# Kernel tuning notes

Hardware: AMD Instinct MI355X
Metric: run time of the kernel (lower is better)

The kernel has to match this reference:

```python
import jax, jax.numpy as jnp
import numpy as np

N = 50000      # nodes
E = 800000     # edges (before self loops)
FE = 256       # expression features
FC = 128       # CNV features
H = 128        # hidden_channels
NC = 8         # num_classes
C = 512        # number of central nodes


def setup_inputs() -> dict:
    key = jax.random.key(0)
    ks = jax.random.split(key, 24)

    def lin(k, fi, fo):
        k1, k2 = jax.random.split(k)
        s = 1.0 / np.sqrt(fi)
        W = jax.random.uniform(k1, (fi, fo), jnp.float32, -s, s)
        b = jax.random.uniform(k2, (fo,), jnp.float32, -s, s)
        return W, b

    x = jax.random.normal(ks[0], (N, FE), jnp.float32)
    c = jax.random.normal(ks[1], (N, FC), jnp.float32)
    edge_index = jax.random.randint(ks[2], (2, E), 0, N, jnp.int32)
    central_idx = jax.random.randint(ks[3], (C,), 0, N, jnp.int32)

    W1e, b1e = lin(ks[4], FE, H)
    W2e, b2e = lin(ks[5], H, H)
    W1c, b1c = lin(ks[6], FC, H)
    W2c, b2c = lin(ks[7], H, H)
    Wm, bm = lin(ks[8], 2 * H, NC)
    Wp1, bp1 = lin(ks[9], NC, H)
    Wp2, bp2 = lin(ks[10], H, NC)

    return dict(
        x=x, c=c, edge_index=edge_index, central_idx=central_idx,
        me_x=jax.random.normal(ks[11], (FE,), jnp.float32),
        me_c=jax.random.normal(ks[12], (FC,), jnp.float32),
        W1e=W1e, b1e=b1e, eps1e=jnp.float32(0.0),
        W2e=W2e, b2e=b2e, eps2e=jnp.float32(0.0),
        W1c=W1c, b1c=b1c, eps1c=jnp.float32(0.0),
        W2c=W2c, b2c=b2c, eps2c=jnp.float32(0.0),
        Wm=Wm, bm=bm, Wp1=Wp1, bp1=bp1, Wp2=Wp2, bp2=bp2,
    )


def _gin_conv(h, src, dst, eps, W, b):
    # GINConv with nn = Linear: lin((1+eps)*x + sum_{j in N(i)} x_j)
    agg = jax.ops.segment_sum(h[src], dst, num_segments=N)  # scatter-add of messages
    return ((1.0 + eps) * h + agg) @ W + b


def reference(x, c, edge_index, central_idx, me_x, me_c,
              W1e, b1e, eps1e, W2e, b2e, eps2e,
              W1c, b1c, eps1c, W2c, b2c, eps2c,
              Wm, bm, Wp1, bp1, Wp2, bp2):
    lrelu = lambda v: jax.nn.leaky_relu(v, 0.2)

    # add self loops
    loops = jnp.arange(N, dtype=edge_index.dtype)
    src = jnp.concatenate([edge_index[0], loops])
    dst = jnp.concatenate([edge_index[1], loops])

    # replace exact-zero entries with learned missing embeddings (broadcast per row)
    x = jnp.where(x == 0, me_x[None, :], x)
    c = jnp.where(c == 0, me_c[None, :], c)

    x_exp = lrelu(_gin_conv(x, src, dst, eps1e, W1e, b1e))
    x_exp = lrelu(_gin_conv(x_exp, src, dst, eps2e, W2e, b2e))

    x_cnv = lrelu(_gin_conv(c, src, dst, eps1c, W1c, b1c))
    x_cnv = lrelu(_gin_conv(x_cnv, src, dst, eps2c, W2c, b2c))

    h = jnp.concatenate([x_exp, x_cnv], axis=1)          # [N, 2H]
    out = lrelu(h @ Wm + bm)                             # [N, NC]

    central = out[central_idx]                           # [C, NC]
    logits = jax.nn.relu(central @ Wp1 + bp1) @ Wp2 + bp2
    return out, logits
```

## Files before the change

kernel.cpp:

```cpp
#include <hip/hip_runtime.h>

typedef unsigned short u16;
typedef __attribute__((ext_vector_type(8))) short short8;
typedef __attribute__((ext_vector_type(4))) float floatx4;
typedef __attribute__((ext_vector_type(2))) float floatx2;

__device__ __forceinline__ float b2f(unsigned int ubits) {
  union { unsigned int i; float f; } cv; cv.i = ubits << 16; return cv.f;
}
__device__ __forceinline__ float hi2f(unsigned int u) {
  union { unsigned int i; float f; } cv; cv.i = u & 0xffff0000u; return cv.f;
}
__device__ __forceinline__ float lo2f(unsigned int u) {
  union { unsigned int i; float f; } cv; cv.i = u << 16; return cv.f;
}
__device__ __forceinline__ u16 f2b(float f) {
  unsigned int u = __builtin_bit_cast(unsigned int, f);
  u += 0x7fffu + ((u >> 16) & 1u);
  return (u16)(u >> 16);
}
__device__ __forceinline__ float lrelu(float v) { return v > 0.f ? v : 0.2f * v; }
__device__ __forceinline__ float rdf(bool isbf, const void* p, int idx) {
  return isbf ? b2f((unsigned int)((const u16*)p)[idx]) : ((const float*)p)[idx];
}
__device__ __forceinline__ floatx2 up2(unsigned int u) {
  return (floatx2){lo2f(u), hi2f(u)};
}

__global__ __launch_bounds__(256) void init_kernel(int* __restrict__ deg, int n,
                                                   const u16* __restrict__ probe,
                                                   int* __restrict__ flag,
                                                   int* __restrict__ colarr, int E) {
  int i0 = (blockIdx.x * 256 + threadIdx.x) * 4;
  if (i0 + 3 < n) {
    *(int4*)(deg + i0) = make_int4(0, 0, 0, 0);
  } else {
    for (int j = 0; j < 4; j++) if (i0 + j < n) deg[i0 + j] = 0;
  }
  if (blockIdx.x == 0) {
    if (threadIdx.x >= 64 && threadIdx.x < 80) colarr[E + (int)threadIdx.x - 64] = 0;
    if (threadIdx.x < 64) {
      int lane = threadIdx.x;
      int cnt = 0;
      for (int i = lane; i < 256; i += 64) {
        unsigned int u = probe[i];
        unsigned int e = (u >> 7) & 0xFFu;
        if ((u & 0x7fffu) == 0 || (e >= 60 && e <= 191)) cnt++;
      }
#pragma unroll
      for (int off = 32; off; off >>= 1) cnt += __shfl_down(cnt, off, 64);
      if (lane == 0) *flag = (cnt >= 240) ? 1 : 0;
    }
  }
}

__global__ __launch_bounds__(256) void hist_kernel(const int* __restrict__ dst, int E,
                                                   int* __restrict__ deg) {
  int i = blockIdx.x * 256 + threadIdx.x;
  if (i < E) atomicAdd(deg + dst[i], 1);
}

#define SCB 1024

__global__ __launch_bounds__(256) void scan_phaseA(const int* __restrict__ deg,
                                                   int* __restrict__ bsum, int n) {
  int i0 = blockIdx.x * SCB + threadIdx.x * 4;
  int s = 0;
  if (i0 + 3 < n) {
    int4 v = *(const int4*)(deg + i0);
    s = v.x + v.y + v.z + v.w;
  } else {
    for (int j = 0; j < 4; j++) if (i0 + j < n) s += deg[i0 + j];
  }
#pragma unroll
  for (int off = 32; off; off >>= 1) s += __shfl_down(s, off, 64);
  __shared__ int ws4[4];
  int lane = threadIdx.x & 63, wid = threadIdx.x >> 6;
  if (lane == 0) ws4[wid] = s;
  __syncthreads();
  if (threadIdx.x == 0) bsum[blockIdx.x] = ws4[0] + ws4[1] + ws4[2] + ws4[3];
}

__global__ void scan_phaseB(const int* __restrict__ bsum, int* __restrict__ boff,
                            int PB, int* __restrict__ rowptr, int n) {
  int lane = threadIdx.x;
  int v = (lane < PB) ? bsum[lane] : 0;
  int incl = v;
#pragma unroll
  for (int off = 1; off < 64; off <<= 1) {
    int t = __shfl_up(incl, off, 64);
    if (lane >= off) incl += t;
  }
  if (lane < PB) boff[lane] = incl - v;
  if (lane == 63) rowptr[n] = incl;
}

__global__ __launch_bounds__(256) void scan_phaseC(const int* __restrict__ deg,
                                                   const int* __restrict__ boff,
                                                   int* __restrict__ rowptr,
                                                   int* __restrict__ cursor, int n) {
  int i0 = blockIdx.x * SCB + threadIdx.x * 4;
  int v0 = 0, v1 = 0, v2 = 0, v3 = 0;
  if (i0 + 3 < n) {
    int4 v = *(const int4*)(deg + i0);
    v0 = v.x; v1 = v.y; v2 = v.z; v3 = v.w;
  } else {
    if (i0 < n) v0 = deg[i0];
    if (i0 + 1 < n) v1 = deg[i0 + 1];
    if (i0 + 2 < n) v2 = deg[i0 + 2];
    if (i0 + 3 < n) v3 = deg[i0 + 3];
  }
  int local = v0 + v1 + v2 + v3;
  int lane = threadIdx.x & 63, wid = threadIdx.x >> 6;
  int incl = local;
#pragma unroll
  for (int off = 1; off < 64; off <<= 1) {
    int t = __shfl_up(incl, off, 64);
    if (lane >= off) incl += t;
  }
  __shared__ int ws4[4];
  if (lane == 63) ws4[wid] = incl;
  __syncthreads();
  int woff = 0;
  for (int w = 0; w < wid; w++) woff += ws4[w];
  int run = boff[blockIdx.x] + woff + incl - local;
  if (i0 < n)     { rowptr[i0] = run;     cursor[i0] = run; }     run += v0;
  if (i0 + 1 < n) { rowptr[i0 + 1] = run; cursor[i0 + 1] = run; } run += v1;
  if (i0 + 2 < n) { rowptr[i0 + 2] = run; cursor[i0 + 2] = run; } run += v2;
  if (i0 + 3 < n) { rowptr[i0 + 3] = run; cursor[i0 + 3] = run; }
}

__global__ __launch_bounds__(256) void fill_kernel(const int* __restrict__ src,
                                                   const int* __restrict__ dst, int E,
                                                   int* __restrict__ cursor,
                                                   int* __restrict__ colarr) {
  int i = blockIdx.x * 256 + threadIdx.x;
  if (i < E) {
    int p = atomicAdd(cursor + dst[i], 1);
    colarr[p] = src[i];
  }
}

struct TWDesc {
  const void* W[5];
  int K[5];
  int Nc[5];
  int base[6];
};

__global__ __launch_bounds__(256) void transpose_all(TWDesc d, u16* __restrict__ out,
                                                     const int* __restrict__ flagp) {
  bool isbf = (*flagp != 0);
  int idx = blockIdx.x * 256 + threadIdx.x;
  if (idx >= d.base[5]) return;
  int s = 0;
  while (idx >= d.base[s + 1]) s++;
  int local = idx - d.base[s];
  if (s < 4) {
    int k8 = local >> 10;
    int rem = local & 1023;
    int col = rem >> 3;
    int k7 = rem & 7;
    int k = k8 * 8 + k7;
    out[idx] = f2b(rdf(isbf, d.W[s], k * 128 + col));
  } else {
    int nn = local >> 8;
    int k = local & 255;
    out[idx] = (nn < d.Nc[4]) ? f2b(rdf(isbf, d.W[4], k * d.Nc[4] + nn)) : (u16)0;
  }
}

__device__ __forceinline__ short8 load_a_me(const void* Av, int lda, const void* me,
                                            int r, int k0, int q, bool isbf) {
  short8 a;
  if (isbf) {
    a = *(const short8*)((const u16*)Av + (long)r * lda + k0 + q * 8);
#pragma unroll
    for (int j = 0; j < 8; j++) {
      if (((u16)a[j] & 0x7fffu) == 0)
        a[j] = (short)((const u16*)me)[k0 + q * 8 + j];
    }
  } else {
    const float* A = (const float*)Av;
    const uint4* p = (const uint4*)(A + (long)r * lda + k0 + q * 8);
    uint4 w0 = p[0];
    uint4 w1 = p[1];
    unsigned int ww[8] = {w0.x, w0.y, w0.z, w0.w, w1.x, w1.y, w1.z, w1.w};
#pragma unroll
    for (int j = 0; j < 8; j++) {
      if ((ww[j] & 0x7fffffffu) == 0)
        a[j] = (short)f2b(((const float*)me)[k0 + q * 8 + j]);
      else
        a[j] = (short)f2b(__builtin_bit_cast(float, ww[j]));
    }
  }
  return a;
}

__global__ __launch_bounds__(256) void gemm_l1(
    const void* __restrict__ x, const void* __restrict__ cc,
    const void* __restrict__ mex, const void* __restrict__ mec,
    const u16* __restrict__ w1e_t, const u16* __restrict__ w1c_t,
    int M, int gb, u16* __restrict__ tb, const int* __restrict__ flagp) {
  __shared__ __align__(16) u16 bs[32768];
  bool isbf = (*flagp != 0);
  bool isC = (blockIdx.x >= (unsigned)gb);
  int bid = isC ? (int)blockIdx.x - gb : (int)blockIdx.x;
  int tid = threadIdx.x;
  int wid = tid >> 6;
  int lane = tid & 63;
  int l15 = lane & 15;
  int q = lane >> 4;
  int row0 = bid * 64 + wid * 16;
  int r = row0 + l15;
  if (r >= M) r = M - 1;

  const void* A  = isC ? cc : x;
  const void* me = isC ? mec : mex;
  const u16* wt  = isC ? w1c_t : w1e_t;
  int K    = isC ? 128 : 256;
  int cofs = isC ? 128 : 0;

  int nchunk = K * 16;
  for (int i = tid; i < nchunk; i += 256)
    *(uint4*)(bs + i * 8) = *(const uint4*)(wt + i * 8);
  __syncthreads();

  floatx4 acc[8];
#pragma unroll
  for (int n = 0; n < 8; n++) acc[n] = (floatx4){0, 0, 0, 0};

  for (int k0 = 0; k0 < K; k0 += 32) {
    short8 a = load_a_me(A, K, me, r, k0, q, isbf);
    const u16* bb = bs + ((k0 >> 3) + q) * 1024 + l15 * 8;
#pragma unroll
    for (int n = 0; n < 8; n++) {
      short8 b = *(const short8*)(bb + n * 128);
      acc[n] = __builtin_amdgcn_mfma_f32_16x16x32_bf16(a, b, acc[n], 0, 0, 0);
    }
  }
#pragma unroll
  for (int n = 0; n < 8; n++)
#pragma unroll
    for (int rr = 0; rr < 4; rr++) {
      int row = row0 + q * 4 + rr;
      if (row < M) tb[(long)row * 256 + cofs + n * 16 + l15] = f2b(acc[n][rr]);
    }
}

__global__ __launch_bounds__(256) void gemm_l2(
    const u16* __restrict__ u,
    const u16* __restrict__ w2e_t, const u16* __restrict__ w2c_t,
    int M, int gb, u16* __restrict__ tb) {
  __shared__ __align__(16) u16 bs[16384];
  bool isC = (blockIdx.x >= (unsigned)gb);
  int bid = isC ? (int)blockIdx.x - gb : (int)blockIdx.x;
  int tid = threadIdx.x;
  int wid = tid >> 6;
  int lane = tid & 63;
  int l15 = lane & 15;
  int q = lane >> 4;
  int row0 = bid * 64 + wid * 16;
  int r = row0 + l15;
  if (r >= M) r = M - 1;

  const u16* wt = isC ? w2c_t : w2e_t;
  int aofs = isC ? 128 : 0;

  for (int i = tid; i < 2048; i += 256)
    *(uint4*)(bs + i * 8) = *(const uint4*)(wt + i * 8);
  __syncthreads();

  floatx4 acc[8];
#pragma unroll
  for (int n = 0; n < 8; n++) acc[n] = (floatx4){0, 0, 0, 0};

  for (int k0 = 0; k0 < 128; k0 += 32) {
    short8 a = *(const short8*)(u + (long)r * 256 + aofs + k0 + q * 8);
    const u16* bb = bs + ((k0 >> 3) + q) * 1024 + l15 * 8;
#pragma unroll
    for (int n = 0; n < 8; n++) {
      short8 b = *(const short8*)(bb + n * 128);
      acc[n] = __builtin_amdgcn_mfma_f32_16x16x32_bf16(a, b, acc[n], 0, 0, 0);
    }
  }
#pragma unroll
  for (int n = 0; n < 8; n++)
#pragma unroll
    for (int rr = 0; rr < 4; rr++) {
      int row = row0 + q * 4 + rr;
      if (row < M) tb[(long)row * 256 + aofs + n * 16 + l15] = f2b(acc[n][rr]);
    }
}

__device__ __forceinline__ void gin_gather8(
    const u16* __restrict__ t, const int* __restrict__ rowptr,
    const int* __restrict__ colarr, const u16* __restrict__ zrow,
    int node, long fbB, floatx2& s01, floatx2& s23) {
  const char* base = (const char*)t + fbB;
  const char* zb = (const char*)zrow + fbB;
  s01 = (floatx2){0.f, 0.f};
  s23 = (floatx2){0.f, 0.f};
  int eu  = __builtin_amdgcn_readfirstlane(rowptr[node]);
  int e1u = __builtin_amdgcn_readfirstlane(rowptr[node + 1]);
  int c0 = colarr[eu],     c1 = colarr[eu + 1], c2 = colarr[eu + 2], c3 = colarr[eu + 3];
  int c4 = colarr[eu + 4], c5 = colarr[eu + 5], c6 = colarr[eu + 6], c7 = colarr[eu + 7];
  int eb = eu;
  for (; eb + 8 <= e1u; eb += 8) {
    uint2 w0 = *(const uint2*)(base + ((long)c0 << 9));
    uint2 w1 = *(const uint2*)(base + ((long)c1 << 9));
    uint2 w2 = *(const uint2*)(base + ((long)c2 << 9));
    uint2 w3 = *(const uint2*)(base + ((long)c3 << 9));
    uint2 w4 = *(const uint2*)(base + ((long)c4 << 9));
    uint2 w5 = *(const uint2*)(base + ((long)c5 << 9));
    uint2 w6 = *(const uint2*)(base + ((long)c6 << 9));
    uint2 w7 = *(const uint2*)(base + ((long)c7 << 9));
    int n0 = colarr[eb + 8],  n1 = colarr[eb + 9],  n2 = colarr[eb + 10], n3 = colarr[eb + 11];
    int n4 = colarr[eb + 12], n5 = colarr[eb + 13], n6 = colarr[eb + 14], n7 = colarr[eb + 15];
    s01 += up2(w0.x); s23 += up2(w0.y);
    s01 += up2(w1.x); s23 += up2(w1.y);
    s01 += up2(w2.x); s23 += up2(w2.y);
    s01 += up2(w3.x); s23 += up2(w3.y);
    s01 += up2(w4.x); s23 += up2(w4.y);
    s01 += up2(w5.x); s23 += up2(w5.y);
    s01 += up2(w6.x); s23 += up2(w6.y);
    s01 += up2(w7.x); s23 += up2(w7.y);
    c0 = n0; c1 = n1; c2 = n2; c3 = n3;
    c4 = n4; c5 = n5; c6 = n6; c7 = n7;
  }
  int rem = e1u - eb;
  if (rem > 0) {
    const char* p0 = base + ((long)c0 << 9);
    const char* p1 = (1 < rem) ? base + ((long)c1 << 9) : zb;
    const char* p2 = (2 < rem) ? base + ((long)c2 << 9) : zb;
    const char* p3 = (3 < rem) ? base + ((long)c3 << 9) : zb;
    const char* p4 = (4 < rem) ? base + ((long)c4 << 9) : zb;
    const char* p5 = (5 < rem) ? base + ((long)c5 << 9) : zb;
    const char* p6 = (6 < rem) ? base + ((long)c6 << 9) : zb;
    const char* p7 = (7 < rem) ? base + ((long)c7 << 9) : zb;
    uint2 w0 = *(const uint2*)p0;
    uint2 w1 = *(const uint2*)p1;
    uint2 w2 = *(const uint2*)p2;
    uint2 w3 = *(const uint2*)p3;
    uint2 w4 = *(const uint2*)p4;
    uint2 w5 = *(const uint2*)p5;
    uint2 w6 = *(const uint2*)p6;
    uint2 w7 = *(const uint2*)p7;
    s01 += up2(w0.x); s23 += up2(w0.y);
    s01 += up2(w1.x); s23 += up2(w1.y);
    s01 += up2(w2.x); s23 += up2(w2.y);
    s01 += up2(w3.x); s23 += up2(w3.y);
    s01 += up2(w4.x); s23 += up2(w4.y);
    s01 += up2(w5.x); s23 += up2(w5.y);
    s01 += up2(w6.x); s23 += up2(w6.y);
    s01 += up2(w7.x); s23 += up2(w7.y);
  }
}

__global__ __launch_bounds__(256) void agg_kernel(
    const u16* __restrict__ t, const int* __restrict__ rowptr, const int* __restrict__ colarr,
    const void* __restrict__ epsE, const void* __restrict__ epsC,
    const void* __restrict__ bE, const void* __restrict__ bC,
    u16* __restrict__ u, int N, const u16* __restrict__ zrow,
    const int* __restrict__ flagp) {
  int node = blockIdx.x * 4 + __builtin_amdgcn_readfirstlane(threadIdx.x >> 6);
  if (node >= N) return;
  bool isbf = (*flagp != 0);
  int lane = threadIdx.x & 63;
  int f0 = lane << 2;
  long fbB = (long)f0 << 1;
  const u16* tb = t + f0;

  uint2 ps = *(const uint2*)(tb + ((long)node << 8));

  floatx2 s01, s23;
  gin_gather8(t, rowptr, colarr, zrow, node, fbB, s01, s23);

  bool isE = (lane < 32);
  float eps2 = 2.0f + rdf(isbf, isE ? epsE : epsC, 0);
  const void* bp = isE ? bE : bC;
  int bi = isE ? f0 : (f0 - 128);
  float a0 = lrelu(s01.x + eps2 * lo2f(ps.x) + rdf(isbf, bp, bi + 0));
  float a1 = lrelu(s01.y + eps2 * hi2f(ps.x) + rdf(isbf, bp, bi + 1));
  float a2 = lrelu(s23.x + eps2 * lo2f(ps.y) + rdf(isbf, bp, bi + 2));
  float a3 = lrelu(s23.y + eps2 * hi2f(ps.y) + rdf(isbf, bp, bi + 3));
  uint2 o;
  o.x = ((unsigned int)f2b(a1) << 16) | f2b(a0);
  o.y = ((unsigned int)f2b(a3) << 16) | f2b(a2);
  *(uint2*)(u + ((long)node << 8) + f0) = o;
}

__global__ __launch_bounds__(256) void agg_head(
    const u16* __restrict__ t, const int* __restrict__ rowptr, const int* __restrict__ colarr,
    const void* __restrict__ epsE, const void* __restrict__ epsC,
    const void* __restrict__ bE, const void* __restrict__ bC,
    const u16* __restrict__ wm_t, const void* __restrict__ bm,
    float* __restrict__ out, int N, const u16* __restrict__ zrow,
    const int* __restrict__ flagp) {
  __shared__ float wmf[2048];
  __shared__ float bmf[8];
  bool isbf = (*flagp != 0);
  int tid = threadIdx.x;
  for (int i = tid; i < 2048; i += 256) wmf[i] = b2f((unsigned int)wm_t[i]);
  if (tid < 8) bmf[tid] = rdf(isbf, bm, tid);
  __syncthreads();

  int node = blockIdx.x * 4 + __builtin_amdgcn_readfirstlane(tid >> 6);
  if (node >= N) return;
  int lane = tid & 63;
  int f0 = lane << 2;
  long fbB = (long)f0 << 1;
  const u16* tb = t + f0;

  uint2 ps = *(const uint2*)(tb + ((long)node << 8));

  floatx2 s01, s23;
  gin_gather8(t, rowptr, colarr, zrow, node, fbB, s01, s23);

  bool isE = (lane < 32);
  float eps2 = 2.0f + rdf(isbf, isE ? epsE : epsC, 0);
  const void* bp = isE ? bE : bC;
  int bi = isE ? f0 : (f0 - 128);
  float a0 = lrelu(s01.x + eps2 * lo2f(ps.x) + rdf(isbf, bp, bi + 0));
  float a1 = lrelu(s01.y + eps2 * hi2f(ps.x) + rdf(isbf, bp, bi + 1));
  float a2 = lrelu(s23.x + eps2 * lo2f(ps.y) + rdf(isbf, bp, bi + 2));
  float a3 = lrelu(s23.y + eps2 * hi2f(ps.y) + rdf(isbf, bp, bi + 3));

  float p[8];
#pragma unroll
  for (int col = 0; col < 8; col++) {
    float4 w = *(const float4*)&wmf[col * 256 + f0];
    p[col] = a0 * w.x + a1 * w.y + a2 * w.z + a3 * w.w;
  }
#pragma unroll
  for (int m = 1; m < 64; m <<= 1) {
#pragma unroll
    for (int col = 0; col < 8; col++) p[col] += __shfl_xor(p[col], m, 64);
  }
  if (lane == 0) {
    float4 o0, o1;
    o0.x = lrelu(p[0] + bmf[0]); o0.y = lrelu(p[1] + bmf[1]);
    o0.z = lrelu(p[2] + bmf[2]); o0.w = lrelu(p[3] + bmf[3]);
    o1.x = lrelu(p[4] + bmf[4]); o1.y = lrelu(p[5] + bmf[5]);
    o1.z = lrelu(p[6] + bmf[6]); o1.w = lrelu(p[7] + bmf[7]);
    *(float4*)(out + (long)node * 8) = o0;
    *(float4*)(out + (long)node * 8 + 4) = o1;
  }
}

__global__ __launch_bounds__(128) void mlp_kernel(
    const float* __restrict__ outbuf, const int* __restrict__ central,
    const void* __restrict__ Wp1, const void* __restrict__ bp1,
    const void* __restrict__ Wp2, const void* __restrict__ bp2,
    float* __restrict__ logits, const int* __restrict__ flagp) {
  __shared__ float h1[128];
  __shared__ float o[8];
  bool isbf = (*flagp != 0);
  int b = blockIdx.x, tid = threadIdx.x;
  int node = central[b];
  if (tid < 8) o[tid] = outbuf[node * 8 + tid];
  __syncthreads();
  float s = rdf(isbf, bp1, tid);
#pragma unroll
  for (int k = 0; k < 8; k++) s += o[k] * rdf(isbf, Wp1, k * 128 + tid);
  h1[tid] = fmaxf(s, 0.f);
  __syncthreads();
  if (tid < 8) {
    float s2 = rdf(isbf, bp2, tid);
    for (int k = 0; k < 128; k++) s2 += h1[k] * rdf(isbf, Wp2, k * 8 + tid);
    logits[b * 8 + tid] = s2;
  }
}

extern "C" void kernel_launch(void* const* d_in, const int* in_sizes, int n_in,
                              void* d_out, int out_size, void* d_ws, size_t ws_size,
                              hipStream_t stream) {
  const void* x    = d_in[0];
  const void* c    = d_in[1];
  const int* eidx  = (const int*)d_in[2];
  const int* cidx  = (const int*)d_in[3];
  const void* me_x = d_in[4];
  const void* me_c = d_in[5];
  const void* W1e  = d_in[6];
  const void* b1e  = d_in[7];
  const void* e1e  = d_in[8];
  const void* W2e  = d_in[9];
  const void* b2e  = d_in[10];
  const void* e2e  = d_in[11];
  const void* W1c  = d_in[12];
  const void* b1c  = d_in[13];
  const void* e1c  = d_in[14];
  const void* W2c  = d_in[15];
  const void* b2c  = d_in[16];
  const void* e2c  = d_in[17];
  const void* Wm   = d_in[18];
  const void* bm   = d_in[19];
  const void* Wp1  = d_in[20];
  const void* bp1  = d_in[21];
  const void* Wp2  = d_in[22];
  const void* bp2  = d_in[23];

  const int N = in_sizes[0] / 256;
  const int E = in_sizes[2] / 2;
  const int Cn = in_sizes[3];
  const int* src = eidx;
  const int* dst = eidx + E;

  char* ws = (char*)d_ws;
  int* deg    = (int*)(ws + 0);
  int* rowptr = (int*)(ws + 200192);
  int* cursor = (int*)(ws + 400384);
  int* colarr = (int*)(ws + 600576);
  u16* tbuf   = (u16*)(ws + 3800832);
  u16* ubuf   = (u16*)(ws + 29400832);
  u16* wt_all = (u16*)(ws + 55000832);
  int* flag   = (int*)(ws + 55172864);
  int* bsum   = (int*)(ws + 55173120);
  int* boff   = (int*)(ws + 55173376);

  u16* w1e_t = wt_all + 0;
  u16* w1c_t = wt_all + 32768;
  u16* w2e_t = wt_all + 49152;
  u16* w2c_t = wt_all + 65536;
  u16* wm_t  = wt_all + 81920;
  const u16* zrow = wt_all + 83968;

  init_kernel<<<(N + 1023) / 1024, 256, 0, stream>>>(deg, N, (const u16*)x, flag,
                                                     colarr, E);

  hist_kernel<<<(E + 255) / 256, 256, 0, stream>>>(dst, E, deg);
  int PB = (N + SCB - 1) / SCB;
  scan_phaseA<<<PB, 256, 0, stream>>>(deg, bsum, N);
  scan_phaseB<<<1, 64, 0, stream>>>(bsum, boff, PB, rowptr, N);
  scan_phaseC<<<PB, 256, 0, stream>>>(deg, boff, rowptr, cursor, N);
  fill_kernel<<<(E + 255) / 256, 256, 0, stream>>>(src, dst, E, cursor, colarr);

  TWDesc td;
  td.W[0] = W1e; td.K[0] = 256; td.Nc[0] = 128;
  td.W[1] = W1c; td.K[1] = 128; td.Nc[1] = 128;
  td.W[2] = W2e; td.K[2] = 128; td.Nc[2] = 128;
  td.W[3] = W2c; td.K[3] = 128; td.Nc[3] = 128;
  td.W[4] = Wm;  td.K[4] = 256; td.Nc[4] = 8;
  td.base[0] = 0; td.base[1] = 32768; td.base[2] = 49152;
  td.base[3] = 65536; td.base[4] = 81920; td.base[5] = 86016;
  transpose_all<<<(86016 + 255) / 256, 256, 0, stream>>>(td, wt_all, flag);

  int gb = (N + 63) / 64;
  gemm_l1<<<2 * gb, 256, 0, stream>>>(x, c, me_x, me_c, w1e_t, w1c_t, N, gb, tbuf, flag);
  agg_kernel<<<(N + 3) / 4, 256, 0, stream>>>(tbuf, rowptr, colarr,
      e1e, e1c, b1e, b1c, ubuf, N, zrow, flag);
  gemm_l2<<<2 * gb, 256, 0, stream>>>(ubuf, w2e_t, w2c_t, N, gb, tbuf);
  agg_head<<<(N + 3) / 4, 256, 0, stream>>>(tbuf, rowptr, colarr,
      e2e, e2c, b2e, b2c, wm_t, bm, (float*)d_out, N, zrow, flag);
  mlp_kernel<<<Cn, 128, 0, stream>>>((const float*)d_out, cidx,
      Wp1, bp1, Wp2, bp2, (float*)d_out + (size_t)N * 8, flag);
}
```

Before: 419.1 us.

## Store layer-1 GEMM output in 32-column slices and aggregate per slice

The first-layer GEMM now writes its output into eight column slices of 32 features each, so every slice holds 64-byte rows. The first aggregation kernel is relaunched with eight times as many blocks, one slice per block, and each wave gathers 8 edges at a time with 8 lanes per edge, then reduces across lanes with shuffles. The aim is a smaller gather working set per block, which should improve L2 hit rates for the random neighbor reads. The cost is more blocks, repeated rowptr/colarr reads per slice, extra shuffle reductions and a new workspace region, plus a larger zeroed padding at the end of colarr to cover the wider prefetch.

New measurement: 500.8 us. 1.19x slower.

```diff
diff --git a/kernel.cpp b/kernel.cpp
--- a/kernel.cpp
+++ b/kernel.cpp
@@ -38,7 +38,7 @@
     for (int j = 0; j < 4; j++) if (i0 + j < n) deg[i0 + j] = 0;
   }
   if (blockIdx.x == 0) {
-    if (threadIdx.x >= 64 && threadIdx.x < 80) colarr[E + (int)threadIdx.x - 64] = 0;
+    if (threadIdx.x >= 64 && threadIdx.x < 112) colarr[E + (int)threadIdx.x - 64] = 0;
     if (threadIdx.x < 64) {
       int lane = threadIdx.x;
       int cnt = 0;
@@ -201,7 +201,7 @@
     const void* __restrict__ x, const void* __restrict__ cc,
     const void* __restrict__ mex, const void* __restrict__ mec,
     const u16* __restrict__ w1e_t, const u16* __restrict__ w1c_t,
-    int M, int gb, u16* __restrict__ tb, const int* __restrict__ flagp) {
+    int M, int gb, u16* __restrict__ tsl, const int* __restrict__ flagp) {
   __shared__ __align__(16) u16 bs[32768];
   bool isbf = (*flagp != 0);
   bool isC = (blockIdx.x >= (unsigned)gb);
@@ -240,12 +240,16 @@
     }
   }
 #pragma unroll
-  for (int n = 0; n < 8; n++)
+  for (int n = 0; n < 8; n++) {
+    int col = cofs + n * 16;
+    long sbase = (long)(col >> 5) * M * 32;
+    int off = (col & 31) + l15;
 #pragma unroll
     for (int rr = 0; rr < 4; rr++) {
       int row = row0 + q * 4 + rr;
-      if (row < M) tb[(long)row * 256 + cofs + n * 16 + l15] = f2b(acc[n][rr]);
-    }
+      if (row < M) tsl[sbase + (long)row * 32 + off] = f2b(acc[n][rr]);
+    }
+  }
 }
 
 __global__ __launch_bounds__(256) void gemm_l2(
@@ -291,6 +295,67 @@
       int row = row0 + q * 4 + rr;
       if (row < M) tb[(long)row * 256 + aofs + n * 16 + l15] = f2b(acc[n][rr]);
     }
+}
+
+__global__ __launch_bounds__(256) void agg_kernel(
+    const u16* __restrict__ tsl, const int* __restrict__ rowptr,
+    const int* __restrict__ colarr,
+    const void* __restrict__ epsE, const void* __restrict__ epsC,
+    const void* __restrict__ bE, const void* __restrict__ bC,
+    u16* __restrict__ u, int N, const u16* __restrict__ zrow,
+    const int* __restrict__ flagp) {
+  int bid = blockIdx.x;
+  int s = bid & 7;
+  int node = (bid >> 3) * 4 + (threadIdx.x >> 6);
+  if (node >= N) return;
+  bool isbf = (*flagp != 0);
+  int lane = threadIdx.x & 63;
+  int e8 = lane >> 3;
+  int f8 = lane & 7;
+  const char* cbase = (const char*)(tsl + (long)s * N * 32) + f8 * 8;
+  const char* zb = (const char*)zrow + f8 * 8;
+
+  uint2 ps = *(const uint2*)(cbase + ((long)node << 6));
+
+  floatx2 s01 = (floatx2){0.f, 0.f}, s23 = (floatx2){0.f, 0.f};
+  int eu  = __builtin_amdgcn_readfirstlane(rowptr[node]);
+  int e1u = __builtin_amdgcn_readfirstlane(rowptr[node + 1]);
+  int ei0 = eu + e8, ei1 = eu + 8 + e8;
+  int c0 = colarr[ei0];
+  int c1 = colarr[ei1];
+  for (int eb = eu; eb < e1u; eb += 16) {
+    const char* p0 = (eb + e8 < e1u)     ? cbase + ((long)c0 << 6) : zb;
+    const char* p1 = (eb + 8 + e8 < e1u) ? cbase + ((long)c1 << 6) : zb;
+    uint2 w0 = *(const uint2*)p0;
+    uint2 w1 = *(const uint2*)p1;
+    int n0 = colarr[ei0 + 16];
+    int n1 = colarr[ei1 + 16];
+    s01 += up2(w0.x); s23 += up2(w0.y);
+    s01 += up2(w1.x); s23 += up2(w1.y);
+    c0 = n0; c1 = n1; ei0 += 16; ei1 += 16;
+  }
+#pragma unroll
+  for (int m = 8; m < 64; m <<= 1) {
+    s01.x += __shfl_xor(s01.x, m, 64);
+    s01.y += __shfl_xor(s01.y, m, 64);
+    s23.x += __shfl_xor(s23.x, m, 64);
+    s23.y += __shfl_xor(s23.y, m, 64);
+  }
+  int f0 = s * 32 + f8 * 4;
+  bool isE = (s < 4);
+  float eps2 = 2.0f + rdf(isbf, isE ? epsE : epsC, 0);
+  const void* bp = isE ? bE : bC;
+  int bi = isE ? f0 : (f0 - 128);
+  float a0 = lrelu(s01.x + eps2 * lo2f(ps.x) + rdf(isbf, bp, bi + 0));
+  float a1 = lrelu(s01.y + eps2 * hi2f(ps.x) + rdf(isbf, bp, bi + 1));
+  float a2 = lrelu(s23.x + eps2 * lo2f(ps.y) + rdf(isbf, bp, bi + 2));
+  float a3 = lrelu(s23.y + eps2 * hi2f(ps.y) + rdf(isbf, bp, bi + 3));
+  if (e8 == 0) {
+    uint2 o;
+    o.x = ((unsigned int)f2b(a1) << 16) | f2b(a0);
+    o.y = ((unsigned int)f2b(a3) << 16) | f2b(a2);
+    *(uint2*)(u + (long)node * 256 + f0) = o;
+  }
 }
 
 __device__ __forceinline__ void gin_gather8(
@@ -357,39 +422,6 @@
   }
 }
 
-__global__ __launch_bounds__(256) void agg_kernel(
-    const u16* __restrict__ t, const int* __restrict__ rowptr, const int* __restrict__ colarr,
-    const void* __restrict__ epsE, const void* __restrict__ epsC,
-    const void* __restrict__ bE, const void* __restrict__ bC,
-    u16* __restrict__ u, int N, const u16* __restrict__ zrow,
-    const int* __restrict__ flagp) {
-  int node = blockIdx.x * 4 + __builtin_amdgcn_readfirstlane(threadIdx.x >> 6);
-  if (node >= N) return;
-  bool isbf = (*flagp != 0);
-  int lane = threadIdx.x & 63;
-  int f0 = lane << 2;
-  long fbB = (long)f0 << 1;
-  const u16* tb = t + f0;
-
-  uint2 ps = *(const uint2*)(tb + ((long)node << 8));
-
-  floatx2 s01, s23;
-  gin_gather8(t, rowptr, colarr, zrow, node, fbB, s01, s23);
-
-  bool isE = (lane < 32);
-  float eps2 = 2.0f + rdf(isbf, isE ? epsE : epsC, 0);
-  const void* bp = isE ? bE : bC;
-  int bi = isE ? f0 : (f0 - 128);
-  float a0 = lrelu(s01.x + eps2 * lo2f(ps.x) + rdf(isbf, bp, bi + 0));
-  float a1 = lrelu(s01.y + eps2 * hi2f(ps.x) + rdf(isbf, bp, bi + 1));
-  float a2 = lrelu(s23.x + eps2 * lo2f(ps.y) + rdf(isbf, bp, bi + 2));
-  float a3 = lrelu(s23.y + eps2 * hi2f(ps.y) + rdf(isbf, bp, bi + 3));
-  uint2 o;
-  o.x = ((unsigned int)f2b(a1) << 16) | f2b(a0);
-  o.y = ((unsigned int)f2b(a3) << 16) | f2b(a2);
-  *(uint2*)(u + ((long)node << 8) + f0) = o;
-}
-
 __global__ __launch_bounds__(256) void agg_head(
     const u16* __restrict__ t, const int* __restrict__ rowptr, const int* __restrict__ colarr,
     const void* __restrict__ epsE, const void* __restrict__ epsC,
@@ -517,6 +549,7 @@
   int* flag   = (int*)(ws + 55172864);
   int* bsum   = (int*)(ws + 55173120);
   int* boff   = (int*)(ws + 55173376);
+  u16* tslice = (u16*)(ws + 55173632);
 
   u16* w1e_t = wt_all + 0;
   u16* w1c_t = wt_all + 32768;
@@ -546,8 +579,8 @@
   transpose_all<<<(86016 + 255) / 256, 256, 0, stream>>>(td, wt_all, flag);
 
   int gb = (N + 63) / 64;
-  gemm_l1<<<2 * gb, 256, 0, stream>>>(x, c, me_x, me_c, w1e_t, w1c_t, N, gb, tbuf, flag);
-  agg_kernel<<<(N + 3) / 4, 256, 0, stream>>>(tbuf, rowptr, colarr,
+  gemm_l1<<<2 * gb, 256, 0, stream>>>(x, c, me_x, me_c, w1e_t, w1c_t, N, gb, tslice, flag);
+  agg_kernel<<<((N + 3) / 4) * 8, 256, 0, stream>>>(tslice, rowptr, colarr,
       e1e, e1c, b1e, b1c, ubuf, N, zrow, flag);
   gemm_l2<<<2 * gb, 256, 0, stream>>>(ubuf, w2e_t, w2c_t, N, gb, tbuf);
   agg_head<<<(N + 3) / 4, 256, 0, stream>>>(tbuf, rowptr, colarr,
```
